# Kernel tuning notes

Measured on AMD Instinct MI355X. Metric: run time of the kernel, lower is better.

## Reference

```python
import jax, jax.numpy as jnp
import numpy as np

T, N, F_IN, F_HID, E = 12, 10000, 128, 128, 160000


def _gcn_norm(src, dst, ew, n):
    # PyG gcn_norm with add_self_loops=False: deg from edge_weight scattered at dst
    deg = jnp.zeros((n,), ew.dtype).at[dst].add(ew)
    dinv = jnp.where(deg > 0, jax.lax.rsqrt(jnp.where(deg > 0, deg, 1.0)), 0.0)
    return dinv[src] * ew * dinv[dst]


def _gcn(x, W, b, src, dst, norm, n):
    h = x @ W                                   # [n, out]
    out = jnp.zeros((n, W.shape[1]), h.dtype).at[dst].add(norm[:, None] * h[src])
    return out + b


def setup_inputs() -> dict:
    key = jax.random.key(0)
    ks = jax.random.split(key, 8)
    s = 1.0 / np.sqrt(F_IN)
    return {
        "x": jax.random.normal(ks[0], (T, N, F_IN), jnp.float32),
        "edge_index": jax.random.randint(ks[1], (2, E), 0, N, dtype=jnp.int64),
        "edge_weight": jax.random.uniform(ks[2], (E,), jnp.float32),
        "W1": jax.random.normal(ks[3], (F_IN, F_HID), jnp.float32) * s,
        "b1": jnp.zeros((F_HID,), jnp.float32),
        "W2": jax.random.normal(ks[4], (F_HID, F_IN), jnp.float32) * s,
        "b2": jnp.zeros((F_IN,), jnp.float32),
        "Wt1": jax.random.normal(ks[5], (F_IN, F_HID), jnp.float32) * s,
        "bt1": jnp.zeros((F_HID,), jnp.float32),
        "Wt2": jax.random.normal(ks[6], (F_HID, F_IN), jnp.float32) * s,
        "bt2": jnp.zeros((F_IN,), jnp.float32),
    }


def reference(x, edge_index, edge_weight, W1, b1, W2, b2, Wt1, bt1, Wt2, bt2):
    src, dst = edge_index[0], edge_index[1]
    norm = _gcn_norm(src, dst, edge_weight, N)

    def spatial(xt):  # [N, F_IN]
        h = jax.nn.relu(_gcn(xt, W1, b1, src, dst, norm, N))
        return _gcn(h, W2, b2, src, dst, norm, N)

    x = jax.vmap(spatial)(x)                    # [T, N, F_IN]

    # temporal block: bidirectional chain edges between consecutive time steps
    xf = x.reshape(T * N, F_IN)
    fwd = jnp.arange((T - 1) * N)
    tsrc = jnp.concatenate([fwd, fwd + N])
    tdst = jnp.concatenate([fwd + N, fwd])
    tw = jnp.ones(tsrc.shape, xf.dtype)
    tnorm = _gcn_norm(tsrc, tdst, tw, T * N)
    h = jax.nn.relu(_gcn(xf, Wt1, bt1, tsrc, tdst, tnorm, T * N))
    xf = _gcn(h, Wt2, bt2, tsrc, tdst, tnorm, T * N)
    x = xf.reshape(T, N, F_IN)

    return jnp.tanh(x)
```

## Files before the change

### kernel.cpp

```cpp
#include <hip/hip_runtime.h>
#include <hip/hip_bf16.h>
#include <hip/hip_fp16.h>

#define T_STEPS 12
#define N_NODES 10000
#define FDIM 128
#define M_ROWS (T_STEPS * N_NODES)

typedef __attribute__((ext_vector_type(8))) short short8v;
typedef __attribute__((ext_vector_type(8))) _Float16 half8v;
typedef __attribute__((ext_vector_type(2))) _Float16 half2v;
typedef __attribute__((ext_vector_type(4))) float f32x4;


__global__ __launch_bounds__(256) void k_count(const int* __restrict__ ei, int* __restrict__ cnt, int E) {
    int e = blockIdx.x * 256 + threadIdx.x;
    if (e < E) atomicAdd(&cnt[ei[E + e]], 1);
}

__global__ __launch_bounds__(256) void k_scan2(const int* __restrict__ cnt, int* __restrict__ rowptr,
                                               int* __restrict__ cursor) {
    __shared__ int part[256];
    int tid = threadIdx.x;
    const int PER = 40;
    int base = tid * PER;
    int s = 0;
#pragma unroll 8
    for (int q = 0; q < PER; ++q) {
        int idx = base + q;
        s += (idx < N_NODES) ? cnt[idx] : 0;
    }
    part[tid] = s;
    __syncthreads();
    for (int off = 1; off < 256; off <<= 1) {
        int v = (tid >= off) ? part[tid - off] : 0;
        __syncthreads();
        part[tid] += v;
        __syncthreads();
    }
    int run = (tid > 0) ? part[tid - 1] : 0;
#pragma unroll 8
    for (int q = 0; q < PER; ++q) {
        int idx = base + q;
        if (idx < N_NODES) {
            rowptr[idx] = run;
            cursor[idx] = run;
            run += cnt[idx];
        }
    }
    if (tid == 255) rowptr[N_NODES] = run;
}

__global__ __launch_bounds__(256) void k_fill(const int* __restrict__ ei, const float* __restrict__ ew,
                                              int* __restrict__ cursor, uint2* __restrict__ epack, int E) {
    int e = blockIdx.x * 256 + threadIdx.x;
    if (e < E) {
        int s = ei[e];
        int d = ei[E + e];
        int slot = atomicAdd(&cursor[d], 1);
        epack[slot] = make_uint2((unsigned)s, __builtin_bit_cast(unsigned, ew[e]));
    }
}

__global__ __launch_bounds__(256) void k_dinv(const int* __restrict__ rowptr, const uint2* __restrict__ epack,
                                              float* __restrict__ dinv) {
    int n = blockIdx.x * 256 + threadIdx.x;
    if (n < N_NODES) {
        int r0 = rowptr[n], r1 = rowptr[n + 1];
        float s = 0.f;
        for (int i = r0; i < r1; ++i) s += __builtin_bit_cast(float, epack[i].y);
        dinv[n] = (s > 0.f) ? rsqrtf(s) : 0.f;
    }
}

__global__ __launch_bounds__(256) void k_scale(const int* __restrict__ rowptr, uint2* __restrict__ epack,
                                               const float* __restrict__ dinv) {
    int n = blockIdx.x * 256 + threadIdx.x;
    if (n < N_NODES) {
        int r0 = rowptr[n], r1 = rowptr[n + 1];
        float dn = dinv[n];
        for (int i = r0; i < r1; ++i) {
            uint2 e = epack[i];
            float v = dn * __builtin_bit_cast(float, e.y) * dinv[e.x];
            epack[i] = make_uint2(e.x * 256u, __builtin_bit_cast(unsigned, v));
        }
    }
}


__global__ __launch_bounds__(256) void k_wsplit4(const float* __restrict__ Wa, const float* __restrict__ Wb,
                                                 const float* __restrict__ Wc, const float* __restrict__ Wd,
                                                 short* __restrict__ base) {
    int wsel = blockIdx.y;
    const float* W = (wsel == 0) ? Wa : (wsel == 1) ? Wb : (wsel == 2) ? Wc : Wd;
    short* Whf = base + (size_t)wsel * 2 * FDIM * FDIM;
    short* Wlf = Whf + FDIM * FDIM;
    int idx = blockIdx.x * 256 + threadIdx.x;
    int k = idx >> 7, col = idx & 127;
    int s = k >> 5, kb = (k >> 3) & 3, j = k & 7;
    float w = W[(size_t)k * FDIM + col];
    _Float16 hi = (_Float16)w;
    _Float16 lo = (_Float16)(w - (float)hi);
    size_t oi = (size_t)(((s * 4 + kb) * 128 + col)) * 8 + j;
    Whf[oi] = __builtin_bit_cast(short, hi);
    Wlf[oi] = __builtin_bit_cast(short, lo);
}


template <typename IN_T, typename OUT_T>
__global__ __launch_bounds__(256) void k_gemm_f16(const IN_T* __restrict__ A,
                                                  const short* __restrict__ Whf,
                                                  const short* __restrict__ Wlf,
                                                  OUT_T* __restrict__ C, int Mrows) {
    int tid = threadIdx.x;
    int wave = tid >> 6, lane = tid & 63;
    int lr = lane & 15, kb = lane >> 4;
    int row0 = blockIdx.x * 64 + wave * 16;

    f32x4 acc[8];
#pragma unroll
    for (int n = 0; n < 8; ++n) acc[n] = (f32x4){0.f, 0.f, 0.f, 0.f};

    int r = row0 + lr;
    if (r > Mrows - 1) r = Mrows - 1;

#pragma unroll
    for (int s = 0; s < 4; ++s) {
        half8v a;
        const IN_T* ap = &A[(size_t)r * FDIM + s * 32 + kb * 8];
        if constexpr (sizeof(IN_T) == 4) {
            float4 x0 = *(const float4*)ap;
            float4 x1 = *(const float4*)(ap + 4);
            a[0] = (_Float16)x0.x; a[1] = (_Float16)x0.y;
            a[2] = (_Float16)x0.z; a[3] = (_Float16)x0.w;
            a[4] = (_Float16)x1.x; a[5] = (_Float16)x1.y;
            a[6] = (_Float16)x1.z; a[7] = (_Float16)x1.w;
        } else {
            a = __builtin_bit_cast(half8v, *(const short8v*)ap);
        }
#pragma unroll
        for (int n = 0; n < 8; ++n) {
            size_t wo = (size_t)(((s * 4 + kb) * 128 + n * 16 + lr)) * 8;
            half8v wh = __builtin_bit_cast(half8v, *(const short8v*)&Whf[wo]);
            half8v wl = __builtin_bit_cast(half8v, *(const short8v*)&Wlf[wo]);
            acc[n] = __builtin_amdgcn_mfma_f32_16x16x32_f16(a, wh, acc[n], 0, 0, 0);
            acc[n] = __builtin_amdgcn_mfma_f32_16x16x32_f16(a, wl, acc[n], 0, 0, 0);
        }
    }
#pragma unroll
    for (int q = 0; q < 4; ++q) {
        int ro = row0 + kb * 4 + q;
        if (ro < Mrows) {
#pragma unroll
            for (int n = 0; n < 8; ++n)
                C[(size_t)ro * FDIM + n * 16 + lr] = (OUT_T)acc[n][q];
        }
    }
}


#define NPB 20
#define NB_HALF 250

__global__ __launch_bounds__(128) void k_aggx(const char* __restrict__ Sbytes,
                                              const int* __restrict__ rowptr,
                                              const uint2* __restrict__ epack,
                                              const float* __restrict__ bias, __half* __restrict__ out,
                                              int do_relu) {
    int bid = blockIdx.x;
    int x = bid & 7;
    int j = bid >> 3;
    int unit = j / NB_HALF;
    int nb = j - unit * NB_HALF;
    int t, n0;
    if (unit == 2) { t = 8 + (x >> 1); n0 = (x & 1) * 5000 + nb * NPB; }
    else           { t = x;            n0 = unit * 5000 + nb * NPB; }

    int wave = threadIdx.x >> 6, lane = threadIdx.x & 63;
    const char* St = Sbytes + (size_t)t * N_NODES * 256;
    unsigned lane4 = (unsigned)lane * 4u;
    float b0 = bias[2 * lane], b1 = bias[2 * lane + 1];

    int nbase = n0 + wave * (NPB / 2);
    for (int nn = 0; nn < NPB / 2; ++nn) {
        int n = nbase + nn;
        int r0 = __builtin_amdgcn_readfirstlane(rowptr[n]);
        int r1 = __builtin_amdgcn_readfirstlane(rowptr[n + 1]);
        float a0 = 0.f, a1 = 0.f;
        int i = r0;
        while (i + 16 <= r1) {
            unsigned sx[16]; float sv[16];
#pragma unroll
            for (int q = 0; q < 16; ++q) {
                uint2 e = epack[i + q];
                sx[q] = e.x;
                sv[q] = __builtin_bit_cast(float, e.y);
            }
            unsigned u[16];
#pragma unroll
            for (int q = 0; q < 16; ++q)
                u[q] = *(const unsigned*)(St + (sx[q] + lane4));
#pragma unroll
            for (int q = 0; q < 16; ++q) {
                half2v h = __builtin_bit_cast(half2v, u[q]);
                a0 = fmaf(sv[q], (float)h[0], a0);
                a1 = fmaf(sv[q], (float)h[1], a1);
            }
            i += 16;
        }
        while (i < r1) {
            unsigned sx[8]; float sv[8];
#pragma unroll
            for (int q = 0; q < 8; ++q) {
                int ii = i + q;
                int ic = (ii < r1) ? ii : r1 - 1;
                uint2 e = epack[ic];
                sx[q] = e.x;
                sv[q] = (ii < r1) ? __builtin_bit_cast(float, e.y) : 0.f;
            }
            unsigned u[8];
#pragma unroll
            for (int q = 0; q < 8; ++q)
                u[q] = *(const unsigned*)(St + (sx[q] + lane4));
#pragma unroll
            for (int q = 0; q < 8; ++q) {
                half2v h = __builtin_bit_cast(half2v, u[q]);
                a0 = fmaf(sv[q], (float)h[0], a0);
                a1 = fmaf(sv[q], (float)h[1], a1);
            }
            i += 8;
        }
        float o0 = a0 + b0, o1 = a1 + b1;
        if (do_relu) { o0 = fmaxf(o0, 0.f); o1 = fmaxf(o1, 0.f); }
        __half2 h = __floats2half2_rn(o0, o1);
        unsigned uo = __builtin_bit_cast(unsigned, h);
        __builtin_nontemporal_store(uo, (unsigned*)&out[((size_t)t * N_NODES + n) * FDIM + 2 * lane]);
    }
}


__device__ __forceinline__ void tagg_core(float2 (&s)[T_STEPS], float b0, float b1,
                                          float2 (&o)[T_STEPS]) {
    const float IS2 = 0.70710678118654752f;
#pragma unroll
    for (int t = 0; t < T_STEPS; ++t) {
        float dt = (t == 0 || t == T_STEPS - 1) ? 1.f : IS2;
        float a0 = 0.f, a1 = 0.f;
        if (t > 0) {
            float dp = (t - 1 == 0) ? 1.f : IS2;
            a0 += dp * s[t - 1].x; a1 += dp * s[t - 1].y;
        }
        if (t < T_STEPS - 1) {
            float dn = (t + 1 == T_STEPS - 1) ? 1.f : IS2;
            a0 += dn * s[t + 1].x; a1 += dn * s[t + 1].y;
        }
        o[t].x = dt * a0 + b0;
        o[t].y = dt * a1 + b1;
    }
}

__global__ __launch_bounds__(256) void k_tagg_relu(const __half2* __restrict__ S2,
                                                   const float* __restrict__ bias,
                                                   __half2* __restrict__ out) {
    int p = blockIdx.x * 256 + threadIdx.x;
    if (p >= N_NODES * 64) return;
    int c2 = p & 63;
    float b0 = bias[2 * c2], b1 = bias[2 * c2 + 1];
    float2 s[T_STEPS], o[T_STEPS];
#pragma unroll
    for (int t = 0; t < T_STEPS; ++t) s[t] = __half22float2(S2[(size_t)t * N_NODES * 64 + p]);
    tagg_core(s, b0, b1, o);
#pragma unroll
    for (int t = 0; t < T_STEPS; ++t) {
        float o0 = fmaxf(o[t].x, 0.f), o1 = fmaxf(o[t].y, 0.f);
        out[(size_t)t * N_NODES * 64 + p] = __floats2half2_rn(o0, o1);
    }
}

__global__ __launch_bounds__(256) void k_tagg_tanh(const __half2* __restrict__ S2,
                                                   const float* __restrict__ bias,
                                                   float* __restrict__ out) {
    int p = blockIdx.x * 256 + threadIdx.x;
    if (p >= N_NODES * 64) return;
    int c2 = p & 63;
    float b0 = bias[2 * c2], b1 = bias[2 * c2 + 1];
    float2 s[T_STEPS], o[T_STEPS];
#pragma unroll
    for (int t = 0; t < T_STEPS; ++t) s[t] = __half22float2(S2[(size_t)t * N_NODES * 64 + p]);
    tagg_core(s, b0, b1, o);
#pragma unroll
    for (int t = 0; t < T_STEPS; ++t) {
        float2 r = make_float2(tanhf(o[t].x), tanhf(o[t].y));
        *(float2*)&out[(size_t)t * N_NODES * FDIM + 2 * (size_t)p] = r;
    }
}


extern "C" void kernel_launch(void* const* d_in, const int* in_sizes, int n_in,
                              void* d_out, int out_size, void* d_ws, size_t ws_size,
                              hipStream_t stream) {
    const float* x   = (const float*)d_in[0];
    const int*   ei  = (const int*)d_in[1];
    const float* ew  = (const float*)d_in[2];
    const float* W1  = (const float*)d_in[3];
    const float* b1  = (const float*)d_in[4];
    const float* W2  = (const float*)d_in[5];
    const float* b2  = (const float*)d_in[6];
    const float* Wt1 = (const float*)d_in[7];
    const float* bt1 = (const float*)d_in[8];
    const float* Wt2 = (const float*)d_in[9];
    const float* bt2 = (const float*)d_in[10];
    float*  outF = (float*)d_out;
    __half* Sh   = (__half*)d_out;
    const int E = in_sizes[2];

    char* w = (char*)d_ws;
    __half* bufH = (__half*)w;
    size_t off   = (size_t)M_ROWS * FDIM * 2;
    __half* S2h  = (__half*)(w + off); off += (size_t)M_ROWS * FDIM * 2;
    int* cnt     = (int*)(w + off); off += (size_t)N_NODES * 4;
    int* rowptr  = (int*)(w + off); off += (size_t)(N_NODES + 1) * 4;
    int* cursor  = (int*)(w + off); off += (size_t)N_NODES * 4;
    uint2* epack = (uint2*)(w + off); off += (size_t)E * 8;
    float* dinv  = (float*)(w + off); off += (size_t)N_NODES * 4;
    short* Wsp   = (short*)(w + off); off += (size_t)8 * FDIM * FDIM * 2;
    const size_t WSZ = (size_t)FDIM * FDIM;
    short* W1h = Wsp;            short* W1l = Wsp + WSZ;
    short* W2h = Wsp + 2 * WSZ;  short* W2l = Wsp + 3 * WSZ;
    short* Wt1h = Wsp + 4 * WSZ; short* Wt1l = Wsp + 5 * WSZ;
    short* Wt2h = Wsp + 6 * WSZ; short* Wt2l = Wsp + 7 * WSZ;

    hipMemsetAsync(cnt, 0, (size_t)N_NODES * 4, stream);
    int eb = (E + 255) / 256;
    int nb = (N_NODES + 255) / 256;
    k_count<<<eb, 256, 0, stream>>>(ei, cnt, E);
    k_scan2<<<1, 256, 0, stream>>>(cnt, rowptr, cursor);
    k_fill<<<eb, 256, 0, stream>>>(ei, ew, cursor, epack, E);
    k_dinv<<<nb, 256, 0, stream>>>(rowptr, epack, dinv);
    k_scale<<<nb, 256, 0, stream>>>(rowptr, epack, dinv);

    dim3 wgrid((FDIM * FDIM) / 256, 4);
    k_wsplit4<<<wgrid, 256, 0, stream>>>(W1, W2, Wt1, Wt2, Wsp);

    int gb = (M_ROWS + 63) / 64;
    int tb = (N_NODES * 64 + 255) / 256;
    int ab = 8 * 3 * NB_HALF;

    k_gemm_f16<float, __half><<<gb, 256, 0, stream>>>(x, W1h, W1l, Sh, M_ROWS);
    k_aggx<<<ab, 128, 0, stream>>>((const char*)Sh, rowptr, epack, b1, bufH, 1);
    k_gemm_f16<__half, __half><<<gb, 256, 0, stream>>>(bufH, W2h, W2l, Sh, M_ROWS);
    k_aggx<<<ab, 128, 0, stream>>>((const char*)Sh, rowptr, epack, b2, bufH, 0);
    k_gemm_f16<__half, __half><<<gb, 256, 0, stream>>>(bufH, Wt1h, Wt1l, Sh, M_ROWS);
    k_tagg_relu<<<tb, 256, 0, stream>>>((const __half2*)Sh, bt1, (__half2*)bufH);
    k_gemm_f16<__half, __half><<<gb, 256, 0, stream>>>(bufH, Wt2h, Wt2l, S2h, M_ROWS);
    k_tagg_tanh<<<tb, 256, 0, stream>>>((const __half2*)S2h, bt2, outF);
}
```

Before: 306.1 us.

## Stage split-fp16 weights in LDS and double rows per wave in GEMM

Result: faster. 270.8 us (-11.5%).

```diff
diff --git a/kernel.cpp b/kernel.cpp
--- a/kernel.cpp
+++ b/kernel.cpp
@@ -11,6 +11,13 @@
 typedef __attribute__((ext_vector_type(8))) _Float16 half8v;
 typedef __attribute__((ext_vector_type(2))) _Float16 half2v;
 typedef __attribute__((ext_vector_type(4))) float f32x4;
+
+__device__ __forceinline__ void gload_lds16(const void* g, void* l) {
+    __builtin_amdgcn_global_load_lds(
+        (const __attribute__((address_space(1))) unsigned int*)g,
+        (__attribute__((address_space(3))) unsigned int*)l,
+        16, 0, 0);
+}
 
 
 __global__ __launch_bounds__(256) void k_count(const int* __restrict__ ei, int* __restrict__ cnt, int E) {
@@ -112,50 +119,74 @@
                                                   const short* __restrict__ Whf,
                                                   const short* __restrict__ Wlf,
                                                   OUT_T* __restrict__ C, int Mrows) {
+    __shared__ short WsL[2 * FDIM * FDIM];
     int tid = threadIdx.x;
     int wave = tid >> 6, lane = tid & 63;
     int lr = lane & 15, kb = lane >> 4;
-    int row0 = blockIdx.x * 64 + wave * 16;
-
-    f32x4 acc[8];
-#pragma unroll
-    for (int n = 0; n < 8; ++n) acc[n] = (f32x4){0.f, 0.f, 0.f, 0.f};
-
-    int r = row0 + lr;
-    if (r > Mrows - 1) r = Mrows - 1;
+    int rbase = blockIdx.x * 128 + wave * 32;
+
+    {
+        const char* srcH = (const char*)Whf;
+        const char* srcL = (const char*)Wlf;
+        char* dst = (char*)WsL;
+#pragma unroll
+        for (int it = 0; it < 8; ++it) {
+            int chunk = (it * 4 + wave) * 1024;
+            gload_lds16(srcH + chunk + lane * 16, dst + chunk);
+            gload_lds16(srcL + chunk + lane * 16, dst + 32768 + chunk);
+        }
+    }
+
+    f32x4 acc[2][8];
+#pragma unroll
+    for (int m = 0; m < 2; ++m)
+#pragma unroll
+        for (int n = 0; n < 8; ++n) acc[m][n] = (f32x4){0.f, 0.f, 0.f, 0.f};
+
+    __syncthreads();
 
 #pragma unroll
     for (int s = 0; s < 4; ++s) {
-        half8v a;
-        const IN_T* ap = &A[(size_t)r * FDIM + s * 32 + kb * 8];
-        if constexpr (sizeof(IN_T) == 4) {
-            float4 x0 = *(const float4*)ap;
-            float4 x1 = *(const float4*)(ap + 4);
-            a[0] = (_Float16)x0.x; a[1] = (_Float16)x0.y;
-            a[2] = (_Float16)x0.z; a[3] = (_Float16)x0.w;
-            a[4] = (_Float16)x1.x; a[5] = (_Float16)x1.y;
-            a[6] = (_Float16)x1.z; a[7] = (_Float16)x1.w;
-        } else {
-            a = __builtin_bit_cast(half8v, *(const short8v*)ap);
+        half8v a[2];
+#pragma unroll
+        for (int m = 0; m < 2; ++m) {
+            int r = rbase + m * 16 + lr;
+            if (r > Mrows - 1) r = Mrows - 1;
+            const IN_T* ap = &A[(size_t)r * FDIM + s * 32 + kb * 8];
+            if constexpr (sizeof(IN_T) == 4) {
+                float4 x0 = *(const float4*)ap;
+                float4 x1 = *(const float4*)(ap + 4);
+                a[m][0] = (_Float16)x0.x; a[m][1] = (_Float16)x0.y;
+                a[m][2] = (_Float16)x0.z; a[m][3] = (_Float16)x0.w;
+                a[m][4] = (_Float16)x1.x; a[m][5] = (_Float16)x1.y;
+                a[m][6] = (_Float16)x1.z; a[m][7] = (_Float16)x1.w;
+            } else {
+                a[m] = __builtin_bit_cast(half8v, *(const short8v*)ap);
+            }
         }
 #pragma unroll
         for (int n = 0; n < 8; ++n) {
-            size_t wo = (size_t)(((s * 4 + kb) * 128 + n * 16 + lr)) * 8;
-            half8v wh = __builtin_bit_cast(half8v, *(const short8v*)&Whf[wo]);
-            half8v wl = __builtin_bit_cast(half8v, *(const short8v*)&Wlf[wo]);
-            acc[n] = __builtin_amdgcn_mfma_f32_16x16x32_f16(a, wh, acc[n], 0, 0, 0);
-            acc[n] = __builtin_amdgcn_mfma_f32_16x16x32_f16(a, wl, acc[n], 0, 0, 0);
-        }
-    }
-#pragma unroll
-    for (int q = 0; q < 4; ++q) {
-        int ro = row0 + kb * 4 + q;
-        if (ro < Mrows) {
-#pragma unroll
-            for (int n = 0; n < 8; ++n)
-                C[(size_t)ro * FDIM + n * 16 + lr] = (OUT_T)acc[n][q];
-        }
-    }
+            int wo = (((s * 4 + kb) * 128 + n * 16 + lr)) * 8;
+            half8v wh = __builtin_bit_cast(half8v, *(const short8v*)&WsL[wo]);
+            half8v wl = __builtin_bit_cast(half8v, *(const short8v*)&WsL[16384 + wo]);
+#pragma unroll
+            for (int m = 0; m < 2; ++m) {
+                acc[m][n] = __builtin_amdgcn_mfma_f32_16x16x32_f16(a[m], wh, acc[m][n], 0, 0, 0);
+                acc[m][n] = __builtin_amdgcn_mfma_f32_16x16x32_f16(a[m], wl, acc[m][n], 0, 0, 0);
+            }
+        }
+    }
+#pragma unroll
+    for (int m = 0; m < 2; ++m)
+#pragma unroll
+        for (int q = 0; q < 4; ++q) {
+            int r = rbase + m * 16 + kb * 4 + q;
+            if (r < Mrows) {
+#pragma unroll
+                for (int n = 0; n < 8; ++n)
+                    C[(size_t)r * FDIM + n * 16 + lr] = (OUT_T)acc[m][n][q];
+            }
+        }
 }
 
 
@@ -342,7 +373,7 @@
     dim3 wgrid((FDIM * FDIM) / 256, 4);
     k_wsplit4<<<wgrid, 256, 0, stream>>>(W1, W2, Wt1, Wt2, Wsp);
 
-    int gb = (M_ROWS + 63) / 64;
+    int gb = (M_ROWS + 127) / 128;
     int tb = (N_NODES * 64 + 255) / 256;
     int ab = 8 * 3 * NB_HALF;
 
```
